# Optimization experiments

Measured on AMD Instinct MI355X. Metric: run time of the kernel, lower is better.

Reference implementation:

```python
import jax, jax.numpy as jnp
import numpy as np

B, N, K, ACT = 8192, 784, 16, 4  # batch, qubits/pixels, Kraus rank, d^2
L = N - 1


def setup_inputs() -> dict:
    key = jax.random.key(0)
    kx, kr, ki = jax.random.split(key, 3)
    X = jax.random.normal(kx, (B, N, 2), dtype=jnp.float32)
    # Random TPCP maps per layer via QR of a (K*4, 4) complex Gaussian (isometry method)
    M = (jax.random.normal(kr, (L, K * ACT, ACT), dtype=jnp.float32)
         + 1j * jax.random.normal(ki, (L, K * ACT, ACT), dtype=jnp.float32))
    Q, _ = jnp.linalg.qr(M)  # (L, K*4, 4), Q^dag Q = I per layer
    Kops = Q.reshape(L, K, ACT, ACT)
    return {
        "X": X,
        "kraus_real": jnp.real(Kops).astype(jnp.float32),
        "kraus_imag": jnp.imag(Kops).astype(jnp.float32),
    }


def _get_rho(x):
    # x: (B, 2) real -> pure-state density matrix (B, 2, 2)
    return jnp.einsum('bi,bj->bij', x, x)


def _tensor_product(r1, r2):
    # (B,2,2) x (B,2,2) -> (B,4,4)
    b = r1.shape[0]
    return jnp.einsum('bij,bkl->bikjl', r1, r2).reshape(b, ACT, ACT)


def _forward_layer(rho, Kl):
    # sum_k K_k rho K_k^dag ; Kl: (K,4,4), rho: (B,4,4)
    return jnp.einsum('kab,nbc,kdc->nad', Kl, rho, jnp.conj(Kl))


def _partial0(rho):
    # trace out qubit 0: (B,4,4) -> (B,2,2)
    b = rho.shape[0]
    return jnp.einsum('nacad->ncd', rho.reshape(b, 2, 2, 2, 2))


def reference(X, kraus_real, kraus_imag):
    kraus = kraus_real + 1j * kraus_imag          # (L, K, 4, 4) complex64
    X = X / jnp.linalg.norm(X, axis=-1, keepdims=True)
    Xc = X.astype(kraus.dtype)
    rho = _tensor_product(_get_rho(Xc[:, 0]), _get_rho(Xc[:, 1]))  # (B,4,4)

    def step(rho, xs):
        Kl, x = xs                                # (K,4,4), (B,2)
        rho = _forward_layer(rho, Kl)
        rho = _tensor_product(_partial0(rho), _get_rho(x))
        return rho, None

    xs = (kraus[:-1], jnp.swapaxes(Xc[:, 2:], 0, 1))  # (L-1,K,4,4), (L-1,B,2)
    rho, _ = jax.lax.scan(step, rho, xs)
    rho = _forward_layer(rho, kraus[-1])
    res = _partial0(rho)[:, 0, 0]                 # (B,) diagonal element, real-valued
    return jnp.real(res)
```

## Files before the change

kernel.cpp:

```cpp
#include <hip/hip_runtime.h>

#define L_LAYERS 783
#define L_PAD    784
#define B_BATCH  8192
#define N_SITES  784
#define K_KRAUS  16

#define SEGF     14
#define GF       56
#define SEGS     28
#define GS       28
#define TPBS     128

__global__ void __launch_bounds__(256)
build_T(const float* __restrict__ kr, const float* __restrict__ ki,
        float* __restrict__ Tc) {
    __shared__ float lr[K_KRAUS * 16];
    __shared__ float li[K_KRAUS * 16];
    __shared__ float gr[48], gi[48];
    int l = blockIdx.x;
    int t = threadIdx.x;
    float* o = Tc + (size_t)l * 48;

    if (l >= L_LAYERS) {
        if (t < 16) {
            int row = t >> 2, col = t & 3;
            o[t]      = (row == col) ? 1.f : 0.f;
            o[16 + t] = 0.f;
            o[32 + t] = 0.f;
        }
        return;
    }

    lr[t] = kr[(size_t)l * 256 + t];
    li[t] = ki[(size_t)l * 256 + t];
    __syncthreads();

    if (t < 192) {
        int e = t >> 2, chunk = t & 3;
        int ci = e >> 4;
        int c = ci >> 1, d = (ci + 1) >> 1;
        int m = (e >> 2) & 3, q = e & 3;
        int i1 = m >> 1, j1 = m & 1, i2 = q >> 1, j2 = q & 1;
        int off1 = c * 4 + 2 * i1 + i2;
        int off2 = d * 4 + 2 * j1 + j2;
        float ar = 0.f, ai = 0.f;
        #pragma unroll
        for (int kk = 0; kk < 4; ++kk) {
            int kbase = (chunk * 4 + kk) * 16;
            #pragma unroll
            for (int a = 0; a < 2; ++a) {
                int x1 = kbase + a * 8 + off1;
                int x2 = kbase + a * 8 + off2;
                float k1r = lr[x1], k1i = li[x1];
                float k2r = lr[x2], k2i = li[x2];
                ar += k1r * k2r + k1i * k2i;
                ai += k1i * k2r - k1r * k2i;
            }
        }
        ar += __shfl_xor(ar, 1); ar += __shfl_xor(ar, 2);
        ai += __shfl_xor(ai, 1); ai += __shfl_xor(ai, 2);
        if (chunk == 0) { gr[e] = ar; gi[e] = ai; }
    }
    __syncthreads();

    if (t < 16) {
        int row = t >> 2, col = t & 3;
        int ci = (row == 0) ? 0 : (row == 1) ? 2 : 1;
        int base = ci * 16;
        float Ur[4], Ui[4];
        #pragma unroll
        for (int q = 0; q < 4; ++q) {
            if (col == 0)      { Ur[q] = gr[base + q];      Ui[q] = gi[base + q]; }
            else if (col == 1) { Ur[q] = gr[base + 12 + q]; Ui[q] = gi[base + 12 + q]; }
            else {
                float t1r = gr[base + 4 + q], t1i = gi[base + 4 + q];
                float t2r = gr[base + 8 + q], t2i = gi[base + 8 + q];
                if (col == 2) { Ur[q] = t1r + t2r;    Ui[q] = t1i + t2i; }
                else          { Ur[q] = -(t1i - t2i); Ui[q] = t1r - t2r; }
            }
        }
        float A, Bc, Cc;
        if (row == 3) { A = Ui[0]; Bc = Ui[1] + Ui[2]; Cc = Ui[3]; }
        else          { A = Ur[0]; Bc = Ur[1] + Ur[2]; Cc = Ur[3]; }
        o[t]      = Cc;
        o[16 + t] = A - Cc;
        o[32 + t] = Bc;
    }
}

__global__ void __launch_bounds__(256, 4)
seg_fused(const float* __restrict__ X, const float* __restrict__ Tc,
          float* __restrict__ P) {
    __shared__ float4 tcs4[SEGF * 12];
    __shared__ float2 xxs[256 * SEGF];
    int t  = threadIdx.x;
    int s  = blockIdx.y;
    int ls = s * SEGF;
    int b0 = blockIdx.x * 256;

    const float4* tg = (const float4*)Tc + (size_t)ls * 12;
    if (t < SEGF * 12) tcs4[t] = tg[t];

    const float2* Xp = (const float2*)X;
    #pragma unroll
    for (int e = 0; e < SEGF; ++e) {
        int idx  = t + e * 256;
        int row  = idx / SEGF;
        int col  = idx - row * SEGF;
        int site = ls + 1 + col;
        site = site < (N_SITES - 1) ? site : (N_SITES - 1);
        float2 xv = Xp[(size_t)(b0 + row) * N_SITES + site];
        float inv = __builtin_amdgcn_rcpf(fmaf(xv.x, xv.x, xv.y * xv.y));
        xxs[row * SEGF + col] = make_float2(xv.x * xv.x * inv, xv.x * xv.y * inv);
    }
    __syncthreads();

    float pA[16], pB[16];
    #pragma unroll
    for (int i = 0; i < 16; ++i) pA[i] = (i % 5 == 0) ? 1.f : 0.f;

#define STEP(SRC, DST, I)                                                       \
    {                                                                           \
        float2 xx = xxs[t * SEGF + (I)];                                        \
        float R[16];                                                            \
        _Pragma("unroll")                                                       \
        for (int r = 0; r < 4; ++r) {                                           \
            float4 cv = tcs4[(I) * 12 + r];                                     \
            float4 dv = tcs4[(I) * 12 + 4 + r];                                 \
            float4 bv = tcs4[(I) * 12 + 8 + r];                                 \
            R[r * 4 + 0] = fmaf(bv.x, xx.y, fmaf(dv.x, xx.x, cv.x));            \
            R[r * 4 + 1] = fmaf(bv.y, xx.y, fmaf(dv.y, xx.x, cv.y));            \
            R[r * 4 + 2] = fmaf(bv.z, xx.y, fmaf(dv.z, xx.x, cv.z));            \
            R[r * 4 + 3] = fmaf(bv.w, xx.y, fmaf(dv.w, xx.x, cv.w));            \
        }                                                                       \
        _Pragma("unroll")                                                       \
        for (int r = 0; r < 4; ++r) {                                           \
            _Pragma("unroll")                                                   \
            for (int cc = 0; cc < 4; ++cc)                                      \
                DST[r * 4 + cc] =                                               \
                    fmaf(R[r * 4 + 0], SRC[cc],                                 \
                    fmaf(R[r * 4 + 1], SRC[4 + cc],                             \
                    fmaf(R[r * 4 + 2], SRC[8 + cc],                             \
                         R[r * 4 + 3] * SRC[12 + cc])));                        \
        }                                                                       \
    }

    #pragma unroll
    for (int i = 0; i < SEGF; i += 2) {
        STEP(pA, pB, i);
        STEP(pB, pA, i + 1);
    }
#undef STEP

    int b = b0 + t;
    #pragma unroll
    for (int i = 0; i < 16; ++i)
        P[((size_t)(s * 16 + i)) * B_BATCH + b] = pA[i];
}

__global__ void __launch_bounds__(256)
combine56(const float* __restrict__ X, const float* __restrict__ P,
          float* __restrict__ out) {
    __shared__ float q[256][17];
    int t = threadIdx.x;
    int j = t >> 5, bl = t & 31;
    int b = blockIdx.x * 32 + bl;

    float qa[16], qb[16];
    #pragma unroll
    for (int i = 0; i < 16; ++i) qa[i] = (i % 5 == 0) ? 1.f : 0.f;

#define CSTEP(SRC, DST, K)                                                      \
    {                                                                           \
        float m[16];                                                            \
        _Pragma("unroll")                                                       \
        for (int i = 0; i < 16; ++i)                                            \
            m[i] = P[((size_t)((j * 7 + (K)) * 16 + i)) * B_BATCH + b];         \
        _Pragma("unroll")                                                       \
        for (int r = 0; r < 4; ++r) {                                           \
            _Pragma("unroll")                                                   \
            for (int cc = 0; cc < 4; ++cc)                                      \
                DST[r * 4 + cc] =                                               \
                    fmaf(m[r * 4 + 0], SRC[cc],                                 \
                    fmaf(m[r * 4 + 1], SRC[4 + cc],                             \
                    fmaf(m[r * 4 + 2], SRC[8 + cc],                             \
                         m[r * 4 + 3] * SRC[12 + cc])));                        \
        }                                                                       \
    }
    CSTEP(qa, qb, 0); CSTEP(qb, qa, 1);
    CSTEP(qa, qb, 2); CSTEP(qb, qa, 3);
    CSTEP(qa, qb, 4); CSTEP(qb, qa, 5);
    CSTEP(qa, qb, 6);
#undef CSTEP

    #pragma unroll
    for (int i = 0; i < 16; ++i) q[t][i] = qb[i];
    __syncthreads();

    if (t < 32) {
        int b2 = blockIdx.x * 32 + t;
        const float2* Xp = (const float2*)X;
        float2 xv = Xp[(size_t)b2 * N_SITES];
        float inv = __builtin_amdgcn_rcpf(fmaf(xv.x, xv.x, xv.y * xv.y));
        float v0 = xv.x * xv.x * inv;
        float v1 = xv.y * xv.y * inv;
        float v2 = xv.x * xv.y * inv;
        float v3 = 0.f;
        #pragma unroll
        for (int jj = 0; jj < 8; ++jj) {
            const float* qq = q[jj * 32 + t];
            float n0 = fmaf(qq[0],  v0, fmaf(qq[1],  v1, fmaf(qq[2],  v2, qq[3]  * v3)));
            float n1 = fmaf(qq[4],  v0, fmaf(qq[5],  v1, fmaf(qq[6],  v2, qq[7]  * v3)));
            float n2 = fmaf(qq[8],  v0, fmaf(qq[9],  v1, fmaf(qq[10], v2, qq[11] * v3)));
            float n3 = fmaf(qq[12], v0, fmaf(qq[13], v1, fmaf(qq[14], v2, qq[15] * v3)));
            v0 = n0; v1 = n1; v2 = n2; v3 = n3;
        }
        out[b2] = v0;
    }
}

__global__ void __launch_bounds__(TPBS)
seg_slow(const float* __restrict__ X, const float* __restrict__ Tc,
         float* __restrict__ P) {
    __shared__ float4 tcs4[SEGS * 12];
    __shared__ float2 xxs[TPBS][SEGS + 1];
    int t  = threadIdx.x;
    int s  = blockIdx.y;
    int ls = s * SEGS;
    int b0 = blockIdx.x * TPBS;

    const float4* tg = (const float4*)Tc + (size_t)ls * 12;
    #pragma unroll
    for (int i = t; i < SEGS * 12; i += TPBS) tcs4[i] = tg[i];

    const float2* Xp = (const float2*)X;
    for (int idx = t; idx < SEGS * TPBS; idx += TPBS) {
        int col  = idx % SEGS;
        int row  = idx / SEGS;
        int site = ls + 1 + col;
        site = site < (N_SITES - 1) ? site : (N_SITES - 1);
        float2 xv = Xp[(size_t)(b0 + row) * N_SITES + site];
        float inv = __builtin_amdgcn_rcpf(fmaf(xv.x, xv.x, xv.y * xv.y));
        xxs[row][col] = make_float2(xv.x * xv.x * inv, xv.x * xv.y * inv);
    }
    __syncthreads();

    float pA[16], pB[16];
    #pragma unroll
    for (int i = 0; i < 16; ++i) pA[i] = (i % 5 == 0) ? 1.f : 0.f;

#define STEP(SRC, DST, I)                                                       \
    {                                                                           \
        float2 xx = xxs[t][I];                                                  \
        float R[16];                                                            \
        _Pragma("unroll")                                                       \
        for (int r = 0; r < 4; ++r) {                                           \
            float4 cv = tcs4[(I) * 12 + r];                                     \
            float4 dv = tcs4[(I) * 12 + 4 + r];                                 \
            float4 bv = tcs4[(I) * 12 + 8 + r];                                 \
            R[r * 4 + 0] = fmaf(bv.x, xx.y, fmaf(dv.x, xx.x, cv.x));            \
            R[r * 4 + 1] = fmaf(bv.y, xx.y, fmaf(dv.y, xx.x, cv.y));            \
            R[r * 4 + 2] = fmaf(bv.z, xx.y, fmaf(dv.z, xx.x, cv.z));            \
            R[r * 4 + 3] = fmaf(bv.w, xx.y, fmaf(dv.w, xx.x, cv.w));            \
        }                                                                       \
        _Pragma("unroll")                                                       \
        for (int r = 0; r < 4; ++r) {                                           \
            _Pragma("unroll")                                                   \
            for (int cc = 0; cc < 4; ++cc)                                      \
                DST[r * 4 + cc] =                                               \
                    fmaf(R[r * 4 + 0], SRC[cc],                                 \
                    fmaf(R[r * 4 + 1], SRC[4 + cc],                             \
                    fmaf(R[r * 4 + 2], SRC[8 + cc],                             \
                         R[r * 4 + 3] * SRC[12 + cc])));                        \
        }                                                                       \
    }

    #pragma unroll
    for (int i = 0; i < SEGS; i += 2) {
        STEP(pA, pB, i);
        STEP(pB, pA, i + 1);
    }
#undef STEP

    int b = b0 + t;
    #pragma unroll
    for (int i = 0; i < 16; ++i)
        P[((size_t)(s * 16 + i)) * B_BATCH + b] = pA[i];
}

__global__ void __launch_bounds__(256)
combine28(const float* __restrict__ X, const float* __restrict__ P,
          float* __restrict__ out) {
    __shared__ float q[256][17];
    int t  = threadIdx.x;
    int j  = t >> 6;
    int bl = t & 63;
    int b  = blockIdx.x * 64 + bl;

    float qa[16], qb[16];
    #pragma unroll
    for (int i = 0; i < 16; ++i) qa[i] = (i % 5 == 0) ? 1.f : 0.f;

#define CSTEP(SRC, DST, K)                                                      \
    {                                                                           \
        float m[16];                                                            \
        _Pragma("unroll")                                                       \
        for (int i = 0; i < 16; ++i)                                            \
            m[i] = P[((size_t)((j * 7 + (K)) * 16 + i)) * B_BATCH + b];         \
        _Pragma("unroll")                                                       \
        for (int r = 0; r < 4; ++r) {                                           \
            _Pragma("unroll")                                                   \
            for (int cc = 0; cc < 4; ++cc)                                      \
                DST[r * 4 + cc] =                                               \
                    fmaf(m[r * 4 + 0], SRC[cc],                                 \
                    fmaf(m[r * 4 + 1], SRC[4 + cc],                             \
                    fmaf(m[r * 4 + 2], SRC[8 + cc],                             \
                         m[r * 4 + 3] * SRC[12 + cc])));                        \
        }                                                                       \
    }
    CSTEP(qa, qb, 0); CSTEP(qb, qa, 1);
    CSTEP(qa, qb, 2); CSTEP(qb, qa, 3);
    CSTEP(qa, qb, 4); CSTEP(qb, qa, 5);
    CSTEP(qa, qb, 6);
#undef CSTEP

    #pragma unroll
    for (int i = 0; i < 16; ++i) q[t][i] = qb[i];
    __syncthreads();

    if (t < 64) {
        int b2 = blockIdx.x * 64 + t;
        const float2* Xp = (const float2*)X;
        float2 xv = Xp[(size_t)b2 * N_SITES];
        float inv = __builtin_amdgcn_rcpf(fmaf(xv.x, xv.x, xv.y * xv.y));
        float v0 = xv.x * xv.x * inv;
        float v1 = xv.y * xv.y * inv;
        float v2 = xv.x * xv.y * inv;
        float v3 = 0.f;
        #pragma unroll
        for (int jj = 0; jj < 4; ++jj) {
            const float* qq = q[jj * 64 + t];
            float n0 = fmaf(qq[0],  v0, fmaf(qq[1],  v1, fmaf(qq[2],  v2, qq[3]  * v3)));
            float n1 = fmaf(qq[4],  v0, fmaf(qq[5],  v1, fmaf(qq[6],  v2, qq[7]  * v3)));
            float n2 = fmaf(qq[8],  v0, fmaf(qq[9],  v1, fmaf(qq[10], v2, qq[11] * v3)));
            float n3 = fmaf(qq[12], v0, fmaf(qq[13], v1, fmaf(qq[14], v2, qq[15] * v3)));
            v0 = n0; v1 = n1; v2 = n2; v3 = n3;
        }
        out[b2] = v0;
    }
}

extern "C" void kernel_launch(void* const* d_in, const int* in_sizes, int n_in,
                              void* d_out, int out_size, void* d_ws, size_t ws_size,
                              hipStream_t stream) {
    const float* X  = (const float*)d_in[0];
    const float* kr = (const float*)d_in[1];
    const float* ki = (const float*)d_in[2];
    float* out = (float*)d_out;

    float* Tc = (float*)d_ws;
    const size_t Tb  = (size_t)L_PAD * 48 * sizeof(float);
    const size_t Pfb = (size_t)GF * 16 * B_BATCH * sizeof(float);

    build_T<<<L_PAD, 256, 0, stream>>>(kr, ki, Tc);

    if (ws_size >= Tb + Pfb) {
        float* P = (float*)((char*)d_ws + Tb);
        dim3 gs(B_BATCH / 256, GF);
        seg_fused<<<gs, 256, 0, stream>>>(X, Tc, P);
        combine56<<<B_BATCH / 32, 256, 0, stream>>>(X, P, out);
    } else {
        float* P = (float*)((char*)d_ws + Tb);
        dim3 gs(B_BATCH / TPBS, GS);
        seg_slow<<<gs, TPBS, 0, stream>>>(X, Tc, P);
        combine28<<<B_BATCH / 64, 256, 0, stream>>>(X, P, out);
    }
}
```

Baseline: 38.49 us.

## Stage X in two halves and read transfer coefficients directly from global memory

The shared-memory staging of the per-layer coefficient table is removed. Each step now reads its 48 coefficients straight from global memory through uniform addresses, which the compiler can turn into scalar loads. The normalized X staging buffer is halved by loading 7 sites at a time in two phases with extra barriers, cutting LDS use per block, which could allow more resident blocks. The cost is a second staging phase and more synchronization.

```diff
diff --git a/kernel.cpp b/kernel.cpp
--- a/kernel.cpp
+++ b/kernel.cpp
@@ -92,48 +92,42 @@
 __global__ void __launch_bounds__(256, 4)
 seg_fused(const float* __restrict__ X, const float* __restrict__ Tc,
           float* __restrict__ P) {
-    __shared__ float4 tcs4[SEGF * 12];
-    __shared__ float2 xxs[256 * SEGF];
+    __shared__ float2 xxs[256 * 7];
     int t  = threadIdx.x;
     int s  = blockIdx.y;
     int ls = s * SEGF;
     int b0 = blockIdx.x * 256;
-
-    const float4* tg = (const float4*)Tc + (size_t)ls * 12;
-    if (t < SEGF * 12) tcs4[t] = tg[t];
-
+    const float* tl0 = Tc + (size_t)ls * 48;
     const float2* Xp = (const float2*)X;
-    #pragma unroll
-    for (int e = 0; e < SEGF; ++e) {
-        int idx  = t + e * 256;
-        int row  = idx / SEGF;
-        int col  = idx - row * SEGF;
-        int site = ls + 1 + col;
-        site = site < (N_SITES - 1) ? site : (N_SITES - 1);
-        float2 xv = Xp[(size_t)(b0 + row) * N_SITES + site];
-        float inv = __builtin_amdgcn_rcpf(fmaf(xv.x, xv.x, xv.y * xv.y));
-        xxs[row * SEGF + col] = make_float2(xv.x * xv.x * inv, xv.x * xv.y * inv);
-    }
-    __syncthreads();
 
     float pA[16], pB[16];
     #pragma unroll
     for (int i = 0; i < 16; ++i) pA[i] = (i % 5 == 0) ? 1.f : 0.f;
 
-#define STEP(SRC, DST, I)                                                       \
-    {                                                                           \
-        float2 xx = xxs[t * SEGF + (I)];                                        \
+#define STAGE(H)                                                                \
+    {                                                                           \
+        _Pragma("unroll")                                                       \
+        for (int e = 0; e < 7; ++e) {                                           \
+            int idx  = t + e * 256;                                \
+            int row  = idx / 7;                                                 \
+            int col  = idx - row * 7;                                           \
+            int site = ls + 1 + (H) * 7 + col;                                  \
+            site = site < (N_SITES - 1) ? site : (N_SITES - 1);                 \
+            float2 xv = Xp[(size_t)(b0 + row) * N_SITES + site];                \
+            float inv = __builtin_amdgcn_rcpf(fmaf(xv.x, xv.x, xv.y * xv.y));   \
+            xxs[row * 7 + col] = make_float2(xv.x * xv.x * inv,                 \
+                                             xv.x * xv.y * inv);                \
+        }                                                                       \
+    }
+
+#define STEP(SRC, DST, I, COL)                                                  \
+    {                                                                           \
+        const float* tl = tl0 + (I) * 48;                \
+        float2 xx = xxs[t * 7 + (COL)];                                         \
         float R[16];                                                            \
         _Pragma("unroll")                                                       \
-        for (int r = 0; r < 4; ++r) {                                           \
-            float4 cv = tcs4[(I) * 12 + r];                                     \
-            float4 dv = tcs4[(I) * 12 + 4 + r];                                 \
-            float4 bv = tcs4[(I) * 12 + 8 + r];                                 \
-            R[r * 4 + 0] = fmaf(bv.x, xx.y, fmaf(dv.x, xx.x, cv.x));            \
-            R[r * 4 + 1] = fmaf(bv.y, xx.y, fmaf(dv.y, xx.x, cv.y));            \
-            R[r * 4 + 2] = fmaf(bv.z, xx.y, fmaf(dv.z, xx.x, cv.z));            \
-            R[r * 4 + 3] = fmaf(bv.w, xx.y, fmaf(dv.w, xx.x, cv.w));            \
-        }                                                                       \
+        for (int e = 0; e < 16; ++e)                                            \
+            R[e] = fmaf(tl[32 + e], xx.y, fmaf(tl[16 + e], xx.x, tl[e]));       \
         _Pragma("unroll")                                                       \
         for (int r = 0; r < 4; ++r) {                                           \
             _Pragma("unroll")                                                   \
@@ -146,12 +140,22 @@
         }                                                                       \
     }
 
-    #pragma unroll
-    for (int i = 0; i < SEGF; i += 2) {
-        STEP(pA, pB, i);
-        STEP(pB, pA, i + 1);
-    }
+    STAGE(0);
+    __syncthreads();
+    STEP(pA, pB, 0, 0); STEP(pB, pA, 1, 1);
+    STEP(pA, pB, 2, 2); STEP(pB, pA, 3, 3);
+    STEP(pA, pB, 4, 4); STEP(pB, pA, 5, 5);
+    STEP(pA, pB, 6, 6);
+    __syncthreads();
+
+    STAGE(1);
+    __syncthreads();
+    STEP(pB, pA, 7, 0);  STEP(pA, pB, 8, 1);
+    STEP(pB, pA, 9, 2);  STEP(pA, pB, 10, 3);
+    STEP(pB, pA, 11, 4); STEP(pA, pB, 12, 5);
+    STEP(pB, pA, 13, 6);
 #undef STEP
+#undef STAGE
 
     int b = b0 + t;
     #pragma unroll
```

Measured after the change: 42.32 us. 1.1x slower.
